# Kernel optimization log

Hardware: AMD Instinct MI355X
Metric: run time of the kernel (lower is better)

## Reference

```python
import jax, jax.numpy as jnp
import numpy as np

N_NODES = 200000
N_EDGES = 800000
N_GRAPHS = 2048
N_SUB = 32768
E_SUB = 131072
F_IN = 38
H0, H1, H2 = 256, 128, 64
BN_EPS = 1e-5


def _l2norm(x):
    n = jnp.sqrt(jnp.sum(x * x, axis=1, keepdims=True))
    return x / jnp.maximum(n, 1e-12)


def _bn(x):
    # fresh nn.BatchNorm1d in training mode: gamma=1, beta=0, biased var
    m = x.mean(0, keepdims=True)
    v = x.var(0, keepdims=True)
    return (x - m) * jax.lax.rsqrt(v + BN_EPS)


def _seg_bn(x, seg, num_seg):
    # per-subgraph BatchNorm (source loops over subgraphs, BN stats per subgraph)
    ones = jnp.ones((x.shape[0],), x.dtype)
    cnt = jnp.maximum(jax.ops.segment_sum(ones, seg, num_seg), 1.0)[:, None]
    m = jax.ops.segment_sum(x, seg, num_seg) / cnt
    v = jax.ops.segment_sum(x * x, seg, num_seg) / cnt - m * m
    return (x - m[seg]) * jax.lax.rsqrt(jnp.maximum(v[seg], 0.0) + BN_EPS)


def _seg_mean(x, seg, num_seg):
    ones = jnp.ones((x.shape[0],), x.dtype)
    cnt = jnp.maximum(jax.ops.segment_sum(ones, seg, num_seg), 1.0)[:, None]
    return jax.ops.segment_sum(x, seg, num_seg) / cnt


def _gcn(x, W, b, src, dst):
    N = x.shape[0]
    h = x @ W
    deg = jnp.ones((N,), x.dtype).at[dst].add(1.0)  # in-degree + self loop
    dinv = jax.lax.rsqrt(deg)
    coef = (dinv[src] * dinv[dst])[:, None]
    agg = jnp.zeros_like(h).at[dst].add(coef * h[src]) + (dinv * dinv)[:, None] * h
    return agg + b


def setup_inputs() -> dict:
    key = jax.random.key(0)
    ks = jax.random.split(key, 40)

    def lin(k, fi, fo):
        return jax.random.normal(k, (fi, fo), jnp.float32) / np.float32(np.sqrt(fi))

    inp = {}
    inp['x'] = jax.random.normal(ks[0], (N_NODES, F_IN), jnp.float32)
    inp['edge_index'] = jax.random.randint(ks[1], (2, N_EDGES), 0, N_NODES)
    inp['batch'] = jnp.sort(jax.random.randint(ks[2], (N_NODES,), 0, N_GRAPHS))
    inp['target_x'] = jax.random.normal(ks[3], (N_GRAPHS, F_IN), jnp.float32)
    inp['pos_x'] = jax.random.normal(ks[4], (N_SUB, F_IN), jnp.float32)
    inp['pos_edge_index'] = jax.random.randint(ks[5], (2, E_SUB), 0, N_SUB)
    inp['pos_batch'] = jnp.sort(jax.random.randint(ks[6], (N_SUB,), 0, N_GRAPHS))
    inp['neg_x'] = jax.random.normal(ks[7], (N_SUB, F_IN), jnp.float32)
    inp['neg_edge_index'] = jax.random.randint(ks[8], (2, E_SUB), 0, N_SUB)
    inp['neg_batch'] = jnp.sort(jax.random.randint(ks[9], (N_SUB,), 0, N_GRAPHS))

    # main GCN encoder
    inp['enc_W0'] = lin(ks[10], F_IN, H0); inp['enc_b0'] = jnp.zeros((H0,), jnp.float32)
    inp['enc_W1'] = lin(ks[11], H0, H1);  inp['enc_b1'] = jnp.zeros((H1,), jnp.float32)
    inp['enc_W2'] = lin(ks[12], H1, H2);  inp['enc_b2'] = jnp.zeros((H2,), jnp.float32)
    # decoder (bias=False)
    inp['dec_W0'] = lin(ks[13], H2, H1)
    inp['dec_W1'] = lin(ks[14], H1, H0)
    inp['dec_W2'] = lin(ks[15], H0, F_IN)
    # node MLP encoder
    inp['node_W0'] = lin(ks[16], F_IN, H0); inp['node_b0'] = jnp.zeros((H0,), jnp.float32)
    inp['node_W1'] = lin(ks[17], H0, H1);  inp['node_b1'] = jnp.zeros((H1,), jnp.float32)
    inp['node_W2'] = lin(ks[18], H1, H2);  inp['node_b2'] = jnp.zeros((H2,), jnp.float32)
    # subgraph GCN encoder (last layer of encode_subgraph reuses self.encoders[-1])
    inp['sub_W0'] = lin(ks[19], F_IN, H0); inp['sub_b0'] = jnp.zeros((H0,), jnp.float32)
    inp['sub_W1'] = lin(ks[20], H0, H1);  inp['sub_b1'] = jnp.zeros((H1,), jnp.float32)
    # classifier
    inp['cls_W0'] = lin(ks[21], H2, H1);  inp['cls_b0'] = jnp.zeros((H1,), jnp.float32)
    inp['cls_W1'] = lin(ks[22], H1, 16);  inp['cls_b1'] = jnp.zeros((16,), jnp.float32)
    inp['cls_W2'] = lin(ks[23], 16, 1);   inp['cls_b2'] = jnp.zeros((1,), jnp.float32)
    return inp


def reference(x, edge_index, batch, target_x, pos_x, pos_edge_index, pos_batch,
              neg_x, neg_edge_index, neg_batch,
              enc_W0, enc_b0, enc_W1, enc_b1, enc_W2, enc_b2,
              dec_W0, dec_W1, dec_W2,
              node_W0, node_b0, node_W1, node_b1, node_W2, node_b2,
              sub_W0, sub_b0, sub_W1, sub_b1,
              cls_W0, cls_b0, cls_W1, cls_b1, cls_W2, cls_b2):
    relu = jax.nn.relu
    src, dst = edge_index[0], edge_index[1]

    # encode: GCN -> ReLU -> BN (x2), GCN, L2 normalize
    h = _bn(relu(_gcn(x, enc_W0, enc_b0, src, dst)))
    h = _bn(relu(_gcn(h, enc_W1, enc_b1, src, dst)))
    z = _l2norm(_gcn(h, enc_W2, enc_b2, src, dst))

    # decode: Linear(no bias) ReLU stack, sigmoid output
    r = relu(z @ dec_W0)
    r = relu(r @ dec_W1)
    x_recon = jax.nn.sigmoid(r @ dec_W2)

    z_pool = _seg_mean(z, batch, N_GRAPHS)

    # encode_node on target node features
    t = _bn(relu(target_x @ node_W0 + node_b0))
    t = _bn(relu(t @ node_W1 + node_b1))
    target_z = _l2norm(t @ node_W2 + node_b2)

    # batched subgraph encoding: GCN stack with per-subgraph BatchNorm;
    # last layer reuses main encoders[-1] weights (as in source encode_subgraph)
    def encode_sub(sx, sei, seg):
        s, d = sei[0], sei[1]
        sh = _seg_bn(relu(_gcn(sx, sub_W0, sub_b0, s, d)), seg, N_GRAPHS)
        sh = _seg_bn(relu(_gcn(sh, sub_W1, sub_b1, s, d)), seg, N_GRAPHS)
        return _l2norm(_gcn(sh, enc_W2, enc_b2, s, d))

    pos_z = encode_sub(pos_x, pos_edge_index, pos_batch)
    pos_pool = _seg_mean(pos_z, pos_batch, N_GRAPHS)
    neg_z = encode_sub(neg_x, neg_edge_index, neg_batch)
    neg_pool = _seg_mean(neg_z, neg_batch, N_GRAPHS)

    # classify negative subgraph pools
    p = relu(neg_pool @ cls_W0 + cls_b0)
    p = relu(p @ cls_W1 + cls_b1)
    neg_pred = jax.nn.sigmoid(p @ cls_W2 + cls_b2)

    return (x_recon, z_pool, target_z, pos_pool, neg_pool, neg_pred)
```

## Files before the change

### kernel.cpp

```cpp
#include <hip/hip_runtime.h>
#include <hip/hip_bf16.h>
#include <math.h>

#define N_NODES  200000
#define N_EDGES  800000
#define N_GRAPHS 2048
#define N_SUB    32768
#define E_SUB    131072
#define F_IN     38
#define H0       256
#define H1       128
#define H2       64
#define BN_EPS   1e-5f

typedef __hip_bfloat16 bf16;
typedef __attribute__((ext_vector_type(8))) short short8;
typedef __attribute__((ext_vector_type(4))) short short4v;
typedef __attribute__((ext_vector_type(4))) float float4v;

static __host__ __device__ inline int cdiv(int a, int b) { return (a + b - 1) / b; }

__device__ inline float ldf(const float* p, size_t i) { return p[i]; }
__device__ inline float ldf(const bf16* p, size_t i)  { return __bfloat162float(p[i]); }
__device__ inline void  stf(float* p, size_t i, float v) { p[i] = v; }
// ... 248 lines not shown
__global__ __launch_bounds__(256) void k_gather6(
    const bf16* __restrict__ h, const float* __restrict__ dinv,
    const int* __restrict__ rowptr, const int* __restrict__ col,
    TO* __restrict__ o, int n, const float* __restrict__ bias, int relu)
{
    const int W = LPR * 8;
    const int NG = 64 / LPR;
    const int g = threadIdx.x / LPR;
    const int c0 = (threadIdx.x % LPR) * 8;
    const int nA = (blockIdx.x * 4 + threadIdx.y) * (2 * NG) + g * 2;
    const int nB = nA + 1;
    if (nA >= n) return;
    const bool okB = nB < n;

    int2 rp = *(const int2*)(rowptr + nA);
    int peB = okB ? rowptr[nB + 1] : rp.y;
    float diA = dinv[nA];
    float diB = okB ? dinv[nB] : 0.f;
    short8 zed = {0, 0, 0, 0, 0, 0, 0, 0};
    short8 slA = *(const short8*)(h + (size_t)nA * W + c0);
    short8 slB = okB ? *(const short8*)(h + (size_t)nB * W + c0) : zed;

    int pA = rp.x, peA = rp.y;
    int pB = rp.y;

    float accA[8], accB[8];
    float qA = diA * diA, qB = diB * diB;
#pragma unroll
    for (int j = 0; j < 8; ++j) {
        accA[j] = qA * bits2f(slA[j]);
        accB[j] = qB * bits2f(slB[j]);
    }

    int sA1 = 0, sB1 = 0;
    float dA0 = 0.f, dB0 = 0.f;
    short8 vA0 = zed, vB0 = zed;
    if (pA < peA) {
        int s0 = col[pA];
        sA1 = (pA + 1 < peA) ? col[pA + 1] : 0;
        dA0 = dinv[s0];
        vA0 = *(const short8*)(h + (size_t)s0 * W + c0);
    }
    if (pB < peB) {
        int s0 = col[pB];
        sB1 = (pB + 1 < peB) ? col[pB + 1] : 0;
        dB0 = dinv[s0];
        vB0 = *(const short8*)(h + (size_t)s0 * W + c0);
    }

    while (__any(pA < peA || pB < peB)) {
        if (pA < peA) {
            int sA2 = (pA + 2 < peA) ? col[pA + 2] : 0;
            short8 vA1 = zed;
            float dA1 = 0.f;
            if (pA + 1 < peA) {
                vA1 = *(const short8*)(h + (size_t)sA1 * W + c0);
                dA1 = dinv[sA1];
            }
            float cf = dA0 * diA;
#pragma unroll
            for (int j = 0; j < 8; ++j) accA[j] += cf * bits2f(vA0[j]);
            vA0 = vA1; dA0 = dA1; sA1 = sA2; ++pA;
        }
        if (pB < peB) {
            int sB2 = (pB + 2 < peB) ? col[pB + 2] : 0;
            short8 vB1 = zed;
            float dB1 = 0.f;
            if (pB + 1 < peB) {
                vB1 = *(const short8*)(h + (size_t)sB1 * W + c0);
                dB1 = dinv[sB1];
            }
            float cf = dB0 * diB;
#pragma unroll
            for (int j = 0; j < 8; ++j) accB[j] += cf * bits2f(vB0[j]);
            vB0 = vB1; dB0 = dB1; sB1 = sB2; ++pB;
        }
    }

    float bv[8];
#pragma unroll
    for (int j = 0; j < 8; ++j) bv[j] = 0.f;
    if (bias) {
        float4 b0 = *(const float4*)(bias + c0);
        float4 b1 = *(const float4*)(bias + c0 + 4);
        bv[0] = b0.x; bv[1] = b0.y; bv[2] = b0.z; bv[3] = b0.w;
        bv[4] = b1.x; bv[5] = b1.y; bv[6] = b1.z; bv[7] = b1.w;
    }

    auto store_row = [&](int node, float* acc) {
        float r[8];
#pragma unroll
        for (int j = 0; j < 8; ++j) {
            r[j] = acc[j] + bv[j];
            if (relu) r[j] = fmaxf(r[j], 0.f);
        }
        size_t off = (size_t)node * W + c0;
        if constexpr (sizeof(TO) == 2) {
            short8 pk;
#pragma unroll
            for (int j = 0; j < 8; ++j) pk[j] = bf16bits(r[j]);
            *(short8*)((bf16*)o + off) = pk;
        } else {
            float4 f0 = {r[0], r[1], r[2], r[3]};
            float4 f1 = {r[4], r[5], r[6], r[7]};
            *(float4*)((float*)o + off) = f0;
            *(float4*)((float*)o + off + 4) = f1;
        }
    };
    store_row(nA, accA);
    if (okB) store_row(nB, accB);
}

template <typename TO>
static void launch_gather6(const bf16* h, const float* dinv, const int* rowptr,
                           const int* col, TO* o, int n, int W,
                           const float* bias, int relu, hipStream_t stream) {
    dim3 b(64, 4);
    if (W == 128)
        k_gather6<TO, 16><<<cdiv(n, 32), b, 0, stream>>>(h, dinv, rowptr, col, o, n,
                                                         bias, relu);
    else
        k_gather6<TO, 8><<<cdiv(n, 64), b, 0, stream>>>(h, dinv, rowptr, col, o, n,
                                                        bias, relu);
}

template <int K, int M, int Mp>
__device__ inline void wpack1(const float* __restrict__ W, bf16* __restrict__ o, int j) {
    int kk = j & 31;
    int rem = j >> 5;
    int ncol = rem % Mp;
    int s = rem / Mp;
    int k = s * 32 + kk;
    float v = (k < K && ncol < M) ? W[(size_t)k * M + ncol] : 0.f;
    o[j] = __float2bfloat16(v);
}

__global__ void k_wpack_all(const float* __restrict__ eW0, const float* __restrict__ eW1,
                            const float* __restrict__ eW2, const float* __restrict__ dW0,
                            const float* __restrict__ dW1, const float* __restrict__ dW2,
                            const float* __restrict__ sW0, const float* __restrict__ sW1,
                            bf16* __restrict__ arena) {
    for (int i = blockIdx.x * 256 + threadIdx.x; i < 159744; i += gridDim.x * 256) {
        if (i < 16384)       wpack1<38, 256, 256>(eW0, arena, i);
        else if (i < 49152)  wpack1<256, 128, 128>(eW1, arena + 16384, i - 16384);
        else if (i < 57344)  wpack1<128, 64, 64>(eW2, arena + 49152, i - 49152);
        else if (i < 65536)  wpack1<64, 128, 128>(dW0, arena + 57344, i - 57344);
        else if (i < 98304)  wpack1<128, 256, 256>(dW1, arena + 65536, i - 65536);
        else if (i < 110592) wpack1<256, 38, 48>(dW2, arena + 98304, i - 98304);
        else if (i < 126976) wpack1<38, 256, 256>(sW0, arena + 110592, i - 110592);
        else                 wpack1<256, 128, 128>(sW1, arena + 126976, i - 126976);
    }
}

template <typename TC, int NT, int BNM>
__global__ __launch_bounds__(256) void k_mfma_gemm(
    const bf16* __restrict__ A, const bf16* __restrict__ Wb,
    TC* __restrict__ C, int n, int SA, int Mp, int M, int MC,
    const float* __restrict__ bias, int act,
    const float* __restrict__ mu, const float* __restrict__ sc,
    const int* __restrict__ seg)
{
    const int lane = threadIdx.x;
    const int wave = threadIdx.y;
    const int row0 = blockIdx.x * 64 + wave * 16;
    const int qr = lane >> 4;
    const int lc = lane & 15;

    float4v acc[NT];
#pragma unroll
    for (int t = 0; t < NT; ++t) acc[t] = (float4v){0.f, 0.f, 0.f, 0.f};

    size_t bnbase = 0;
    if (BNM == 2) bnbase = (size_t)seg[row0 + lc] * SA;

    const int S = SA >> 5;
    const bf16* arow = A + (size_t)(row0 + lc) * SA + qr * 8;
    const bf16* wrow = Wb + (size_t)lc * 32 + qr * 8;

    for (int s = 0; s < S; ++s) {
        short8 af = *(const short8*)(arow + s * 32);
        if (BNM != 0) {
            int kb = s * 32 + qr * 8;
            const float* mp = mu + bnbase + kb;
            const float* sp = sc + bnbase + kb;
            float4 m0 = *(const float4*)mp, m1 = *(const float4*)(mp + 4);
            float4 s0 = *(const float4*)sp, s1 = *(const float4*)(sp + 4);
            float av[8];
#pragma unroll
            for (int j = 0; j < 8; ++j) av[j] = bits2f(af[j]);
            av[0] = (av[0] - m0.x) * s0.x; av[1] = (av[1] - m0.y) * s0.y;
            av[2] = (av[2] - m0.z) * s0.z; av[3] = (av[3] - m0.w) * s0.w;
            av[4] = (av[4] - m1.x) * s1.x; av[5] = (av[5] - m1.y) * s1.y;
            av[6] = (av[6] - m1.z) * s1.z; av[7] = (av[7] - m1.w) * s1.w;
#pragma unroll
            for (int j = 0; j < 8; ++j) af[j] = bf16bits(av[j]);
        }
#pragma unroll
        for (int t = 0; t < NT; ++t) {
            short8 bfr = *(const short8*)(wrow + ((size_t)s * Mp + t * 16) * 32);
            acc[t] = __builtin_amdgcn_mfma_f32_16x16x32_bf16(bfr, af, acc[t], 0, 0, 0);
        }
    }

    const int row = row0 + lc;
#pragma unroll
    for (int t = 0; t < NT; ++t) {
        int c0 = t * 16 + qr * 4;
        if (c0 >= M) continue;
        float v[4];
#pragma unroll
        for (int r = 0; r < 4; ++r) v[r] = acc[t][r];
        if (bias) {
            if (c0 + 3 < M) {
                float4 bv = *(const float4*)(bias + c0);
                v[0] += bv.x; v[1] += bv.y; v[2] += bv.z; v[3] += bv.w;
            } else {
#pragma unroll
                for (int r = 0; r < 4; ++r) if (c0 + r < M) v[r] += bias[c0 + r];
            }
        }
#pragma unroll
        for (int r = 0; r < 4; ++r) {
            if (act == 1) v[r] = fmaxf(v[r], 0.f);
            else if (act == 2) v[r] = 1.f / (1.f + expf(-v[r]));
        }
        if (c0 + 3 < M) {
            if constexpr (sizeof(TC) == 2) {
                short4v pk = {bf16bits(v[0]), bf16bits(v[1]), bf16bits(v[2]), bf16bits(v[3])};
                *(short4v*)((bf16*)C + (size_t)row * MC + c0) = pk;
            } else {
                stf2((float*)C, ((size_t)row * MC + c0) >> 1, make_float2(v[0], v[1]));
                stf2((float*)C, ((size_t)row * MC + c0 + 2) >> 1, make_float2(v[2], v[3]));
            }
        } else {
#pragma unroll
            for (int r = 0; r < 4; ++r)
                if (c0 + r < M) stf(C, (size_t)row * MC + c0 + r, v[r]);
        }
    }
}

template <typename TC, int BNM>
static void launch_mfma(const bf16* A, const bf16* Wb, TC* C, int n, int SA,
                        int Mp, int M, int MC, const float* bias, int act,
                        const float* mu, const float* sc, const int* seg,
                        hipStream_t stream) {
    dim3 b(64, 4);
    int g = n / 64;
    if (Mp == 256)      k_mfma_gemm<TC, 16, BNM><<<g, b, 0, stream>>>(A, Wb, C, n, SA, Mp, M, MC, bias, act, mu, sc, seg);
    else if (Mp == 128) k_mfma_gemm<TC, 8, BNM><<<g, b, 0, stream>>>(A, Wb, C, n, SA, Mp, M, MC, bias, act, mu, sc, seg);
    else if (Mp == 64)  k_mfma_gemm<TC, 4, BNM><<<g, b, 0, stream>>>(A, Wb, C, n, SA, Mp, M, MC, bias, act, mu, sc, seg);
    else                k_mfma_gemm<TC, 3, BNM><<<g, b, 0, stream>>>(A, Wb, C, n, SA, Mp, M, MC, bias, act, mu, sc, seg);
}

__global__ __launch_bounds__(256) void k_decoder(
    const bf16* __restrict__ zb, const bf16* __restrict__ dW0b,
    const bf16* __restrict__ dW1b, const bf16* __restrict__ dW2b,
    float* __restrict__ xrec, int n)
{
    __shared__ __attribute__((aligned(16))) char lds[4][12288];
    const int lane = threadIdx.x;
    const int wave = threadIdx.y;
    const int lc = lane & 15, qr = lane >> 4;
    const int row0 = blockIdx.x * 64 + wave * 16;
    char* r1 = lds[wave];
    char* r2 = lds[wave] + 4096;
    const int swz = (lc & 7) << 4;

    float4v a1[8];
#pragma unroll
    for (int t = 0; t < 8; ++t) a1[t] = (float4v){0.f, 0.f, 0.f, 0.f};
    const bf16* arow = zb + (size_t)(row0 + lc) * 64 + qr * 8;
#pragma unroll
    for (int s = 0; s < 2; ++s) {
        short8 af = *(const short8*)(arow + s * 32);
#pragma unroll
        for (int t = 0; t < 8; ++t) {
            short8 wf = *(const short8*)(dW0b + ((size_t)(s * 128 + t * 16 + lc)) * 32 + qr * 8);
            a1[t] = __builtin_amdgcn_mfma_f32_16x16x32_bf16(wf, af, a1[t], 0, 0, 0);
        }
    }
#pragma unroll
    for (int t = 0; t < 8; ++t) {
        short4v pk = {bf16bits(fmaxf(a1[t][0], 0.f)), bf16bits(fmaxf(a1[t][1], 0.f)),
                      bf16bits(fmaxf(a1[t][2], 0.f)), bf16bits(fmaxf(a1[t][3], 0.f))};
        int off = lc * 256 + t * 32 + qr * 8;
        *(short4v*)(r1 + (off ^ swz)) = pk;
    }

    float4v a2[16];
#pragma unroll
    for (int t = 0; t < 16; ++t) a2[t] = (float4v){0.f, 0.f, 0.f, 0.f};
#pragma unroll
    for (int s = 0; s < 4; ++s) {
        int off = lc * 256 + s * 64 + qr * 16;
        short8 af = *(const short8*)(r1 + (off ^ swz));
#pragma unroll
        for (int t = 0; t < 16; ++t) {
            short8 wf = *(const short8*)(dW1b + ((size_t)(s * 256 + t * 16 + lc)) * 32 + qr * 8);
            a2[t] = __builtin_amdgcn_mfma_f32_16x16x32_bf16(wf, af, a2[t], 0, 0, 0);
        }
    }
#pragma unroll
    for (int t = 0; t < 16; ++t) {
        short4v pk = {bf16bits(fmaxf(a2[t][0], 0.f)), bf16bits(fmaxf(a2[t][1], 0.f)),
                      bf16bits(fmaxf(a2[t][2], 0.f)), bf16bits(fmaxf(a2[t][3], 0.f))};
        int off = lc * 512 + t * 32 + qr * 8;
        *(short4v*)(r2 + (off ^ swz)) = pk;
    }

    float4v a3[3];
#pragma unroll
    for (int t = 0; t < 3; ++t) a3[t] = (float4v){0.f, 0.f, 0.f, 0.f};
#pragma unroll
    for (int s = 0; s < 8; ++s) {
        int off = lc * 512 + s * 64 + qr * 16;
        short8 af = *(const short8*)(r2 + (off ^ swz));
#pragma unroll
        for (int t = 0; t < 3; ++t) {
            short8 wf = *(const short8*)(dW2b + ((size_t)(s * 48 + t * 16 + lc)) * 32 + qr * 8);
            a3[t] = __builtin_amdgcn_mfma_f32_16x16x32_bf16(wf, af, a3[t], 0, 0, 0);
        }
    }
    float* orow = xrec + (size_t)(row0 + lc) * 38;
#pragma unroll
    for (int t = 0; t < 3; ++t) {
        int c0 = t * 16 + qr * 4;
        float v0 = 1.f / (1.f + expf(-a3[t][0]));
        float v1 = 1.f / (1.f + expf(-a3[t][1]));
        float v2 = 1.f / (1.f + expf(-a3[t][2]));
        float v3 = 1.f / (1.f + expf(-a3[t][3]));
        if (c0 + 1 < 38) *(float2*)(orow + c0) = make_float2(v0, v1);
        if (c0 + 3 < 38) *(float2*)(orow + c0 + 2) = make_float2(v2, v3);
    }
}

template <typename TA, typename TC, int NJ>
__global__ __launch_bounds__(256) void k_gemm(
    const TA* __restrict__ A, const float* __restrict__ W,
    TC* __restrict__ C, int n, int K, int M,
    const float* __restrict__ bias, int act,
    const float* __restrict__ mu, const float* __restrict__ sc)
{
    __shared__ float alds[64 * 32];
    __shared__ float wlds[32 * 256];
    const int l = threadIdx.x;
    const int wy = threadIdx.y;
    const int tid = wy * 64 + l;
    const int row0 = blockIdx.x * 64;

    float acc[16][NJ];
#pragma unroll
    for (int r = 0; r < 16; ++r)
#pragma unroll
        for (int j = 0; j < NJ; ++j) acc[r][j] = 0.f;

    int cidx[NJ]; bool jval[NJ];
#pragma unroll
    for (int j = 0; j < NJ; ++j) {
        cidx[j] = l + 64 * j;
        jval[j] = cidx[j] < M;
    }

    for (int k0 = 0; k0 < K; k0 += 32) {
        int kt = min(32, K - k0);
        __syncthreads();
        for (int i = tid; i < 64 * 32; i += 256) {
            int r = i >> 5, kk = i & 31;
            int row = row0 + r, k = k0 + kk;
            float v = (row < n && k < K) ? ldf(A, (size_t)row * K + k) : 0.f;
            if (mu && k < K) v = (v - mu[k]) * sc[k];
            alds[i] = v;
        }
        for (int i = tid; i < kt * M; i += 256)
            wlds[i] = W[(size_t)k0 * M + i];
        if (kt < 32)
            for (int i = kt * M + tid; i < 32 * M; i += 256) wlds[i] = 0.f;
        __syncthreads();

#pragma unroll 2
        for (int kkg = 0; kkg < 8; ++kkg) {
            float wv[4][NJ];
#pragma unroll
            for (int q = 0; q < 4; ++q)
#pragma unroll
                for (int j = 0; j < NJ; ++j)
                    wv[q][j] = jval[j] ? wlds[(kkg * 4 + q) * M + cidx[j]] : 0.f;
#pragma unroll
            for (int rr = 0; rr < 16; ++rr) {
                const float4* arow = (const float4*)&alds[(wy * 16 + rr) * 32];
                float4 av = arow[kkg];
#pragma unroll
                for (int j = 0; j < NJ; ++j) {
                    acc[rr][j] += av.x * wv[0][j];
                    acc[rr][j] += av.y * wv[1][j];
                    acc[rr][j] += av.z * wv[2][j];
                    acc[rr][j] += av.w * wv[3][j];
                }
            }
        }
    }

#pragma unroll
    for (int rr = 0; rr < 16; ++rr) {
        int row = row0 + wy * 16 + rr;
// ... 61 lines not shown
    if (c < M) {
        float m = sum[c] / (float)n;
        float v = fmaxf(sumsq[c] / (float)n - m * m, 0.f);
        sum[c] = m;
        sumsq[c] = rsqrtf(v + BN_EPS);
    }
}

template <int CPL>
__global__ __launch_bounds__(256) void k_segbn(
    const bf16* __restrict__ x, const int* __restrict__ gstart, int nseg,
    float* __restrict__ mu, float* __restrict__ sc)
{
    const int M = 64 * CPL;
    int s = blockIdx.x * 4 + threadIdx.y;
    if (s >= nseg) return;
    int l = threadIdx.x;
    int gs = gstart[s], ge = gstart[s + 1];
    float sum[CPL], sq[CPL];
#pragma unroll
    for (int j = 0; j < CPL; ++j) { sum[j] = 0.f; sq[j] = 0.f; }
    for (int r = gs; r < ge; ++r) {
        const bf16* px = x + (size_t)r * M + l * CPL;
        if constexpr (CPL == 4) {
            short4v v4 = *(const short4v*)px;
#pragma unroll
            for (int j = 0; j < 4; ++j) {
                float v = bits2f(v4[j]);
                sum[j] += v; sq[j] += v * v;
            }
        } else {
            __hip_bfloat162 v2 = *(const __hip_bfloat162*)px;
            float v0 = __bfloat162float(v2.x), v1 = __bfloat162float(v2.y);
            sum[0] += v0; sq[0] += v0 * v0;
            sum[1] += v1; sq[1] += v1 * v1;
        }
    }
    float c = fmaxf((float)(ge - gs), 1.f);
#pragma unroll
    for (int j = 0; j < CPL; ++j) {
        float m = sum[j] / c;
        float v = fmaxf(sq[j] / c - m * m, 0.f);
        mu[(size_t)s * M + l * CPL + j] = m;
        sc[(size_t)s * M + l * CPL + j] = rsqrtf(v + BN_EPS);
    }
}

__global__ __launch_bounds__(256) void k_pool(
    const float* __restrict__ z, const int* __restrict__ gstart, int nseg,
    float* __restrict__ o)
{
    int s = blockIdx.x * 4 + threadIdx.y;
    if (s >= nseg) return;
    int l = threadIdx.x;
    int gs = gstart[s], ge = gstart[s + 1];
    float acc = 0.f;
    for (int r = gs; r < ge; ++r) acc += z[(size_t)r * 64 + l];
    o[(size_t)s * 64 + l] = acc / fmaxf((float)(ge - gs), 1.f);
}

__global__ __launch_bounds__(256) void k_l2pool(
    const float* __restrict__ zs, const int* __restrict__ gstart, int nseg,
    float* __restrict__ o)
{
    int s = blockIdx.x * 4 + threadIdx.y;
    if (s >= nseg) return;
    int l = threadIdx.x;
    int gs = gstart[s], ge = gstart[s + 1];
    float acc = 0.f;
    for (int r = gs; r < ge; ++r) {
        float v = zs[(size_t)r * 64 + l];
        float ss = v * v;
        for (int off = 32; off > 0; off >>= 1) ss += __shfl_xor(ss, off, 64);
        acc += v / fmaxf(sqrtf(ss), 1e-12f);
    }
    o[(size_t)s * 64 + l] = acc / fmaxf((float)(ge - gs), 1.f);
}

__global__ void k_l2norm2(float* __restrict__ x, bf16* __restrict__ xb, int n) {
    int row = blockIdx.x * 4 + threadIdx.y;
    if (row >= n) return;
    int l = threadIdx.x;
    float v = x[(size_t)row * 64 + l];
    float ss = v * v;
    for (int o = 32; o > 0; o >>= 1) ss += __shfl_xor(ss, o, 64);
    float r = v / fmaxf(sqrtf(ss), 1e-12f);
    x[(size_t)row * 64 + l] = r;
    if (xb) xb[(size_t)row * 64 + l] = __float2bfloat16(r);
}

template <typename TA, typename TC>
static void launch_gemm(const TA* A, const float* W, TC* C, int n, int K, int M,
                        const float* bias, int act, const float* mu, const float* sc,
                        hipStream_t stream) {
    dim3 b(64, 4);
    int g = cdiv(n, 64);
    int nj = (M + 63) >> 6;
    if (nj >= 4)      k_gemm<TA, TC, 4><<<g, b, 0, stream>>>(A, W, C, n, K, M, bias, act, mu, sc);
    else if (nj == 2) k_gemm<TA, TC, 2><<<g, b, 0, stream>>>(A, W, C, n, K, M, bias, act, mu, sc);
    else              k_gemm<TA, TC, 1><<<g, b, 0, stream>>>(A, W, C, n, K, M, bias, act, mu, sc);
}

extern "C" void kernel_launch(void* const* d_in, const int* in_sizes, int n_in,
                              void* d_out, int out_size, void* d_ws, size_t ws_size,
                              hipStream_t stream) {
    const float* x        = (const float*)d_in[0];
    const int*   ei       = (const int*)  d_in[1];
    const int*   batch    = (const int*)  d_in[2];
    const float* target_x = (const float*)d_in[3];
    const float* pos_x    = (const float*)d_in[4];
    const int*   pos_ei   = (const int*)  d_in[5];
    const int*   pos_b    = (const int*)  d_in[6];
    const float* neg_x    = (const float*)d_in[7];
    const int*   neg_ei   = (const int*)  d_in[8];
    const int*   neg_b    = (const int*)  d_in[9];
    const float* enc_W0 = (const float*)d_in[10]; const float* enc_b0 = (const float*)d_in[11];
    const float* enc_W1 = (const float*)d_in[12]; const float* enc_b1 = (const float*)d_in[13];
    const float* enc_W2 = (const float*)d_in[14]; const float* enc_b2 = (const float*)d_in[15];
    const float* dec_W0 = (const float*)d_in[16];
    const float* dec_W1 = (const float*)d_in[17];
    const float* dec_W2 = (const float*)d_in[18];
    const float* node_W0 = (const float*)d_in[19]; const float* node_b0 = (const float*)d_in[20];
    const float* node_W1 = (const float*)d_in[21]; const float* node_b1 = (const float*)d_in[22];
    const float* node_W2 = (const float*)d_in[23]; const float* node_b2 = (const float*)d_in[24];
    const float* sub_W0 = (const float*)d_in[25]; const float* sub_b0 = (const float*)d_in[26];
    const float* sub_W1 = (const float*)d_in[27]; const float* sub_b1 = (const float*)d_in[28];
    const float* cls_W0 = (const float*)d_in[29]; const float* cls_b0 = (const float*)d_in[30];
    const float* cls_W1 = (const float*)d_in[31]; const float* cls_b1 = (const float*)d_in[32];
    const float* cls_W2 = (const float*)d_in[33]; const float* cls_b2 = (const float*)d_in[34];

    float* out = (float*)d_out;
    const size_t OFF_XREC  = 0;
    const size_t OFF_ZPOOL = (size_t)N_NODES * F_IN;
    const size_t OFF_TZ    = OFF_ZPOOL + (size_t)N_GRAPHS * H2;
    const size_t OFF_PPOOL = OFF_TZ    + (size_t)N_GRAPHS * H2;
    const size_t OFF_NPOOL = OFF_PPOOL + (size_t)N_GRAPHS * H2;
    const size_t OFF_PRED  = OFF_NPOOL + (size_t)N_GRAPHS * H2;

    char* wsp = (char*)d_ws;
    auto alloc = [&](size_t nfloats) -> float* {
        float* p = (float*)wsp;
        wsp += ((nfloats + 63) / 64) * 64 * sizeof(float);
        return p;
    };
    float* R1     = alloc((size_t)N_NODES * 128);
    float* R2     = alloc((size_t)N_NODES * 128);
    float* dinv   = alloc(N_NODES);
    int*   cnt    = (int*)alloc(N_NODES);
    int*   rowptr = (int*)alloc(N_NODES + 1);
    int*   bsum   = (int*)alloc(1024);
    int*   ccol   = (int*)alloc(N_EDGES);
    float* ssum   = alloc(256);
    float* ssumsq = alloc(256);
    bf16*  wpk    = (bf16*)alloc(80 * 1024);
    (void)ws_size; (void)in_sizes; (void)n_in; (void)out_size;

    bf16* eW0b = wpk;
    bf16* eW1b = eW0b + 16384;
    bf16* eW2b = eW1b + 32768;
    bf16* dW0b = eW2b + 8192;
    bf16* dW1b = dW0b + 8192;
    bf16* dW2b = dW1b + 32768;
    bf16* sW0b = dW2b + 12288;
    bf16* sW1b = sW0b + 16384;

    float* tailf    = R2 + (size_t)16 * 1024 * 1024;
    float* segsumM  = tailf;
    float* segsumqM = tailf + (size_t)1048576;
    float* mx       = tailf + (size_t)2097152;
    int*   msrc     = (int*)(mx + (size_t)2 * N_SUB * F_IN);
    int*   mdst     = msrc + 2 * E_SUB;
    int*   mb       = mdst + 2 * E_SUB;
    int*   gstartM  = mb + 2 * N_SUB;
    int*   gstart2k = gstartM + 4112;

    dim3 b64x4(64, 4);
    auto zero = [&](void* p, size_t nfloats) {
        k_zero<<<cdiv((int)nfloats, 256), 256, 0, stream>>>((float*)p, (int)nfloats);
    };

    k_wpack_all<<<624, 256, 0, stream>>>(enc_W0, enc_W1, enc_W2, dec_W0, dec_W1,
                                         dec_W2, sub_W0, sub_W1, wpk);

    auto build_graph = [&](const int* srcp, const int* dstp, int n, int e) {
        zero(cnt, n);
        k_count<<<cdiv(e, 256), 256, 0, stream>>>(dstp, cnt, e);
        k_dinv<<<cdiv(n, 256), 256, 0, stream>>>(cnt, dinv, n);
        int nb = cdiv(n, 256);
        k_scan_sum<<<nb, 256, 0, stream>>>(cnt, bsum, n);
        k_scan_top<<<1, 1024, 0, stream>>>(bsum, nb);
        k_scan_apply<<<nb, 256, 0, stream>>>(cnt, bsum, rowptr, n);
        zero(cnt, n);
        k_fill<<<cdiv(e, 256), 256, 0, stream>>>(srcp, dstp, rowptr, cnt, ccol, e);
    };

    auto bn_stats = [&](auto* xx, int n, int M) {
        zero(ssum, 512);
        int rpb = 256 / (M >> 3);
        int g = min(320, cdiv(n, rpb));
        k_bn_stats8<<<g, 256, 0, stream>>>(xx, n, M, ssum, ssumsq);
        k_bn_fin<<<1, 256, 0, stream>>>(ssum, ssumsq, n, M);
    };

    build_graph(ei, ei + N_EDGES, N_NODES, N_EDGES);

    bf16* Y0 = (bf16*)R2;
    launch_gather<float, bf16>(x, dinv, rowptr, ccol, Y0, N_NODES, F_IN, 64,
                               nullptr, 0, stream);
    bf16* a0 = (bf16*)R1;
    launch_mfma<bf16, 0>(Y0, eW0b, a0, N_NODES, 64, 256, H0, H0, enc_b0, 1,
                         nullptr, nullptr, nullptr, stream);
    bn_stats(a0, N_NODES, H0);

    bf16* G1 = (bf16*)R2;
    launch_mfma<bf16, 1>(a0, eW1b, G1, N_NODES, 256, 128, H1, H1, nullptr, 0,
                         ssum, ssumsq, nullptr, stream);
    bf16* a1 = (bf16*)R1;
    launch_gather6<bf16>(G1, dinv, rowptr, ccol, a1, N_NODES, 128, enc_b1, 1, stream);
    bn_stats(a1, N_NODES, H1);

    bf16* G2 = (bf16*)R2;
    launch_mfma<bf16, 1>(a1, eW2b, G2, N_NODES, 128, 64, H2, H2, nullptr, 0,
                         ssum, ssumsq, nullptr, stream);
    float* z  = R1;
    bf16*  zb = (bf16*)(R1 + (size_t)N_NODES * 64);
    launch_gather6<float>(G2, dinv, rowptr, ccol, z, N_NODES, 64, enc_b2, 0, stream);
    k_l2norm2<<<cdiv(N_NODES, 4), b64x4, 0, stream>>>(z, zb, N_NODES);

    k_gbound<<<cdiv(N_NODES, 256), 256, 0, stream>>>(batch, N_NODES, N_GRAPHS, gstart2k);
    k_pool<<<cdiv(N_GRAPHS, 4), b64x4, 0, stream>>>(z, gstart2k, N_GRAPHS,
                                                    out + OFF_ZPOOL);

    k_decoder<<<N_NODES / 64, b64x4, 0, stream>>>(zb, dW0b, dW1b, dW2b,
                                                  out + OFF_XREC, N_NODES);

    float* t0 = R2;
    launch_gemm<float, float>(target_x, node_W0, t0, N_GRAPHS, F_IN, H0, node_b0, 1,
                              nullptr, nullptr, stream);
    bn_stats(t0, N_GRAPHS, H0);
    float* t1 = R1;
    launch_gemm<float, float>(t0, node_W1, t1, N_GRAPHS, H0, H1, node_b1, 1,
                              ssum, ssumsq, stream);
    bn_stats(t1, N_GRAPHS, H1);
    launch_gemm<float, float>(t1, node_W2, out + OFF_TZ, N_GRAPHS, H1, H2, node_b2, 0,
                              ssum, ssumsq, stream);
    k_l2norm2<<<cdiv(N_GRAPHS, 4), b64x4, 0, stream>>>(out + OFF_TZ, nullptr, N_GRAPHS);

    k_merge<<<2048, 256, 0, stream>>>(pos_x, neg_x, pos_ei, neg_ei, pos_b, neg_b,
                                      mx, msrc, mdst, mb);
    const int NS2 = 2 * N_SUB, ES2 = 2 * E_SUB, NG2 = 2 * N_GRAPHS;
    build_graph(msrc, mdst, NS2, ES2);
    k_gbound<<<cdiv(NS2, 256), 256, 0, stream>>>(mb, NS2, NG2, gstartM);

    bf16* Ys = (bf16*)R2;
    launch_gather<float, bf16>(mx, dinv, rowptr, ccol, Ys, NS2, F_IN, 64,
                               nullptr, 0, stream);
    bf16* as0 = (bf16*)R1;
    launch_mfma<bf16, 0>(Ys, sW0b, as0, NS2, 64, 256, H0, H0, sub_b0, 1,
                         nullptr, nullptr, nullptr, stream);
    k_segbn<4><<<cdiv(NG2, 4), b64x4, 0, stream>>>(as0, gstartM, NG2,
                                                   segsumM, segsumqM);

    bf16* Gs1 = (bf16*)R2;
    launch_mfma<bf16, 2>(as0, sW1b, Gs1, NS2, 256, 128, H1, H1, nullptr, 0,
                         segsumM, segsumqM, mb, stream);
    bf16* as1 = (bf16*)R1;
    launch_gather6<bf16>(Gs1, dinv, rowptr, ccol, as1, NS2, 128, sub_b1, 1, stream);
    k_segbn<2><<<cdiv(NG2, 4), b64x4, 0, stream>>>(as1, gstartM, NG2,
                                                   segsumM, segsumqM);

    bf16* Gs2 = (bf16*)R2;
    launch_mfma<bf16, 2>(as1, eW2b, Gs2, NS2, 128, 64, H2, H2, nullptr, 0,
                         segsumM, segsumqM, mb, stream);
    float* zs = R1;
    launch_gather6<float>(Gs2, dinv, rowptr, ccol, zs, NS2, 64, enc_b2, 0, stream);
    k_l2pool<<<cdiv(NG2, 4), b64x4, 0, stream>>>(zs, gstartM, NG2, out + OFF_PPOOL);

    float* c1 = R2;
    launch_gemm<float, float>(out + OFF_NPOOL, cls_W0, c1, N_GRAPHS, H2, H1, cls_b0, 1,
                              nullptr, nullptr, stream);
    float* c2 = R1;
    launch_gemm<float, float>(c1, cls_W1, c2, N_GRAPHS, H1, 16, cls_b1, 1,
                              nullptr, nullptr, stream);
    launch_gemm<float, float>(c2, cls_W2, out + OFF_PRED, N_GRAPHS, 16, 1, cls_b2, 2,
                              nullptr, nullptr, stream);
}
```

Baseline: 1.271 ms.

## Fold BatchNorm into GEMM weights and pipeline multi-tile MFMA GEMM

Result: slower. 1.334 ms (+5.0%).

```diff
diff --git a/kernel.cpp b/kernel.cpp
--- a/kernel.cpp
+++ b/kernel.cpp
@@ -424,79 +424,110 @@
     }
 }
 
-template <typename TC, int NT, int BNM>
+template <int K, int M, int Mp>
+__global__ void k_wfold(const float* __restrict__ W, const float* __restrict__ mu,
+                        const float* __restrict__ sc, bf16* __restrict__ Wb,
+                        float* __restrict__ bout) {
+    const int tot = (K / 32) * Mp * 32;
+    for (int i = blockIdx.x * 256 + threadIdx.x; i < tot; i += gridDim.x * 256) {
+        int kk = i & 31;
+        int rem = i >> 5;
+        int ncol = rem % Mp;
+        int s = rem / Mp;
+        int k = s * 32 + kk;
+        float v = (k < K && ncol < M) ? sc[k] * W[(size_t)k * M + ncol] : 0.f;
+        Wb[i] = __float2bfloat16(v);
+    }
+    if (blockIdx.x == 0 && threadIdx.x < M) {
+        int j = threadIdx.x;
+        float s = 0.f;
+        for (int k = 0; k < K; ++k) s -= mu[k] * sc[k] * W[(size_t)k * M + j];
+        bout[j] = s;
+    }
+}
+
+template <typename TC, int NT, int S, int BNM, int TPB>
 __global__ __launch_bounds__(256) void k_mfma_gemm(
     const bf16* __restrict__ A, const bf16* __restrict__ Wb,
-    TC* __restrict__ C, int n, int SA, int Mp, int M, int MC,
+    TC* __restrict__ C, int ntiles, int M, int MC,
     const float* __restrict__ bias, int act,
     const float* __restrict__ mu, const float* __restrict__ sc,
     const int* __restrict__ seg)
 {
+    const int SA = S * 32;
+    const int Mp = NT * 16;
     const int lane = threadIdx.x;
     const int wave = threadIdx.y;
-    const int row0 = blockIdx.x * 64 + wave * 16;
     const int qr = lane >> 4;
     const int lc = lane & 15;
-
-    float4v acc[NT];
-#pragma unroll
-    for (int t = 0; t < NT; ++t) acc[t] = (float4v){0.f, 0.f, 0.f, 0.f};
-
-    size_t bnbase = 0;
-    if (BNM == 2) bnbase = (size_t)seg[row0 + lc] * SA;
-
-    const int S = SA >> 5;
-    const bf16* arow = A + (size_t)(row0 + lc) * SA + qr * 8;
-    const bf16* wrow = Wb + (size_t)lc * 32 + qr * 8;
-
-    for (int s = 0; s < S; ++s) {
-        short8 af = *(const short8*)(arow + s * 32);
-        if (BNM != 0) {
-            int kb = s * 32 + qr * 8;
-            const float* mp = mu + bnbase + kb;
-            const float* sp = sc + bnbase + kb;
-            float4 m0 = *(const float4*)mp, m1 = *(const float4*)(mp + 4);
-            float4 s0 = *(const float4*)sp, s1 = *(const float4*)(sp + 4);
-            float av[8];
-#pragma unroll
-            for (int j = 0; j < 8; ++j) av[j] = bits2f(af[j]);
-            av[0] = (av[0] - m0.x) * s0.x; av[1] = (av[1] - m0.y) * s0.y;
-            av[2] = (av[2] - m0.z) * s0.z; av[3] = (av[3] - m0.w) * s0.w;
-            av[4] = (av[4] - m1.x) * s1.x; av[5] = (av[5] - m1.y) * s1.y;
-            av[6] = (av[6] - m1.z) * s1.z; av[7] = (av[7] - m1.w) * s1.w;
-#pragma unroll
-            for (int j = 0; j < 8; ++j) af[j] = bf16bits(av[j]);
-        }
+    const int tile0 = blockIdx.x * TPB;
+    const int ntl = min(TPB, ntiles - tile0);
+    const bf16* wbase = Wb + (size_t)lc * 32 + qr * 8;
+
+    short8 cur[S], nxt[S];
+    {
+        const bf16* ar = A + (size_t)(tile0 * 64 + wave * 16 + lc) * SA + qr * 8;
+#pragma unroll
+        for (int s = 0; s < S; ++s) cur[s] = *(const short8*)(ar + s * 32);
+    }
+
+    for (int it = 0; it < ntl; ++it) {
+        const int row0 = (tile0 + it) * 64 + wave * 16;
+        if (it + 1 < ntl) {
+            const bf16* ar = A + (size_t)(row0 + 64 + lc) * SA + qr * 8;
+#pragma unroll
+            for (int s = 0; s < S; ++s) nxt[s] = *(const short8*)(ar + s * 32);
+        }
+        if (BNM == 2) {
+            size_t bnbase = (size_t)seg[row0 + lc] * SA;
+#pragma unroll
+            for (int s = 0; s < S; ++s) {
+                int kb = s * 32 + qr * 8;
+                const float* mp = mu + bnbase + kb;
+                const float* sp = sc + bnbase + kb;
+                float4 m0 = *(const float4*)mp, m1 = *(const float4*)(mp + 4);
+                float4 s0 = *(const float4*)sp, s1 = *(const float4*)(sp + 4);
+                float av[8];
+#pragma unroll
+                for (int j = 0; j < 8; ++j) av[j] = bits2f(cur[s][j]);
+                av[0] = (av[0] - m0.x) * s0.x; av[1] = (av[1] - m0.y) * s0.y;
+                av[2] = (av[2] - m0.z) * s0.z; av[3] = (av[3] - m0.w) * s0.w;
+                av[4] = (av[4] - m1.x) * s1.x; av[5] = (av[5] - m1.y) * s1.y;
+                av[6] = (av[6] - m1.z) * s1.z; av[7] = (av[7] - m1.w) * s1.w;
+#pragma unroll
+                for (int j = 0; j < 8; ++j) cur[s][j] = bf16bits(av[j]);
+            }
+        }
+
+        float4v acc[NT];
+#pragma unroll
+        for (int t = 0; t < NT; ++t) acc[t] = (float4v){0.f, 0.f, 0.f, 0.f};
+#pragma unroll
+        for (int s = 0; s < S; ++s) {
+#pragma unroll
+            for (int t = 0; t < NT; ++t) {
+                short8 wf = *(const short8*)(wbase + ((size_t)s * Mp + t * 16) * 32);
+                acc[t] = __builtin_amdgcn_mfma_f32_16x16x32_bf16(wf, cur[s], acc[t], 0, 0, 0);
+            }
+        }
+
+        const int row = row0 + lc;
 #pragma unroll
         for (int t = 0; t < NT; ++t) {
-            short8 bfr = *(const short8*)(wrow + ((size_t)s * Mp + t * 16) * 32);
-            acc[t] = __builtin_amdgcn_mfma_f32_16x16x32_bf16(bfr, af, acc[t], 0, 0, 0);
-        }
-    }
-
-    const int row = row0 + lc;
-#pragma unroll
-    for (int t = 0; t < NT; ++t) {
-        int c0 = t * 16 + qr * 4;
-        if (c0 >= M) continue;
-        float v[4];
-#pragma unroll
-        for (int r = 0; r < 4; ++r) v[r] = acc[t][r];
-        if (bias) {
-            if (c0 + 3 < M) {
+            int c0 = t * 16 + qr * 4;
+            if (c0 >= M) continue;
+            float v[4];
+#pragma unroll
+            for (int r = 0; r < 4; ++r) v[r] = acc[t][r];
+            if (bias) {
                 float4 bv = *(const float4*)(bias + c0);
                 v[0] += bv.x; v[1] += bv.y; v[2] += bv.z; v[3] += bv.w;
-            } else {
-#pragma unroll
-                for (int r = 0; r < 4; ++r) if (c0 + r < M) v[r] += bias[c0 + r];
             }
-        }
-#pragma unroll
-        for (int r = 0; r < 4; ++r) {
-            if (act == 1) v[r] = fmaxf(v[r], 0.f);
-            else if (act == 2) v[r] = 1.f / (1.f + expf(-v[r]));
-        }
-        if (c0 + 3 < M) {
+#pragma unroll
+            for (int r = 0; r < 4; ++r) {
+                if (act == 1) v[r] = fmaxf(v[r], 0.f);
+                else if (act == 2) v[r] = 1.f / (1.f + expf(-v[r]));
+            }
             if constexpr (sizeof(TC) == 2) {
                 short4v pk = {bf16bits(v[0]), bf16bits(v[1]), bf16bits(v[2]), bf16bits(v[3])};
                 *(short4v*)((bf16*)C + (size_t)row * MC + c0) = pk;
@@ -504,11 +535,9 @@
                 stf2((float*)C, ((size_t)row * MC + c0) >> 1, make_float2(v[0], v[1]));
                 stf2((float*)C, ((size_t)row * MC + c0 + 2) >> 1, make_float2(v[2], v[3]));
             }
-        } else {
-#pragma unroll
-            for (int r = 0; r < 4; ++r)
-                if (c0 + r < M) stf(C, (size_t)row * MC + c0 + r, v[r]);
-        }
+        }
+#pragma unroll
+        for (int s = 0; s < S; ++s) cur[s] = nxt[s];
     }
 }
 
@@ -518,11 +547,24 @@
                         const float* mu, const float* sc, const int* seg,
                         hipStream_t stream) {
     dim3 b(64, 4);
-    int g = n / 64;
-    if (Mp == 256)      k_mfma_gemm<TC, 16, BNM><<<g, b, 0, stream>>>(A, Wb, C, n, SA, Mp, M, MC, bias, act, mu, sc, seg);
-    else if (Mp == 128) k_mfma_gemm<TC, 8, BNM><<<g, b, 0, stream>>>(A, Wb, C, n, SA, Mp, M, MC, bias, act, mu, sc, seg);
-    else if (Mp == 64)  k_mfma_gemm<TC, 4, BNM><<<g, b, 0, stream>>>(A, Wb, C, n, SA, Mp, M, MC, bias, act, mu, sc, seg);
-    else                k_mfma_gemm<TC, 3, BNM><<<g, b, 0, stream>>>(A, Wb, C, n, SA, Mp, M, MC, bias, act, mu, sc, seg);
+    int ntiles = n / 64;
+    if (ntiles >= 2000) {
+        int g = cdiv(ntiles, 4);
+        if (SA == 64 && Mp == 256)
+            k_mfma_gemm<TC, 16, 2, BNM, 4><<<g, b, 0, stream>>>(A, Wb, C, ntiles, M, MC, bias, act, mu, sc, seg);
+        else if (SA == 256 && Mp == 128)
+            k_mfma_gemm<TC, 8, 8, BNM, 4><<<g, b, 0, stream>>>(A, Wb, C, ntiles, M, MC, bias, act, mu, sc, seg);
+        else if (SA == 128 && Mp == 64)
+            k_mfma_gemm<TC, 4, 4, BNM, 4><<<g, b, 0, stream>>>(A, Wb, C, ntiles, M, MC, bias, act, mu, sc, seg);
+    } else {
+        int g = cdiv(ntiles, 2);
+        if (SA == 64 && Mp == 256)
+            k_mfma_gemm<TC, 16, 2, BNM, 2><<<g, b, 0, stream>>>(A, Wb, C, ntiles, M, MC, bias, act, mu, sc, seg);
+        else if (SA == 256 && Mp == 128)
+            k_mfma_gemm<TC, 8, 8, BNM, 2><<<g, b, 0, stream>>>(A, Wb, C, ntiles, M, MC, bias, act, mu, sc, seg);
+        else if (SA == 128 && Mp == 64)
+            k_mfma_gemm<TC, 4, 4, BNM, 2><<<g, b, 0, stream>>>(A, Wb, C, ntiles, M, MC, bias, act, mu, sc, seg);
+    }
 }
 
 __global__ __launch_bounds__(256) void k_decoder(
@@ -890,7 +932,8 @@
     int*   ccol   = (int*)alloc(N_EDGES);
     float* ssum   = alloc(256);
     float* ssumsq = alloc(256);
-    bf16*  wpk    = (bf16*)alloc(80 * 1024);
+    bf16*  wpk    = (bf16*)alloc(101 * 1024);
+    float* bfold  = alloc(256);
     (void)ws_size; (void)in_sizes; (void)n_in; (void)out_size;
 
     bf16* eW0b = wpk;
@@ -901,6 +944,8 @@
     bf16* dW2b = dW1b + 32768;
     bf16* sW0b = dW2b + 12288;
     bf16* sW1b = sW0b + 16384;
+    bf16* fW1b = sW1b + 32768;
+    bf16* fW2b = fW1b + 32768;
 
     float* tailf    = R2 + (size_t)16 * 1024 * 1024;
     float* segsumM  = tailf;
@@ -935,7 +980,7 @@
     auto bn_stats = [&](auto* xx, int n, int M) {
         zero(ssum, 512);
         int rpb = 256 / (M >> 3);
-        int g = min(320, cdiv(n, rpb));
+        int g = min(512, cdiv(n, rpb));
         k_bn_stats8<<<g, 256, 0, stream>>>(xx, n, M, ssum, ssumsq);
         k_bn_fin<<<1, 256, 0, stream>>>(ssum, ssumsq, n, M);
     };
@@ -949,17 +994,19 @@
     launch_mfma<bf16, 0>(Y0, eW0b, a0, N_NODES, 64, 256, H0, H0, enc_b0, 1,
                          nullptr, nullptr, nullptr, stream);
     bn_stats(a0, N_NODES, H0);
+    k_wfold<256, 128, 128><<<128, 256, 0, stream>>>(enc_W1, ssum, ssumsq, fW1b, bfold);
 
     bf16* G1 = (bf16*)R2;
-    launch_mfma<bf16, 1>(a0, eW1b, G1, N_NODES, 256, 128, H1, H1, nullptr, 0,
-                         ssum, ssumsq, nullptr, stream);
+    launch_mfma<bf16, 0>(a0, fW1b, G1, N_NODES, 256, 128, H1, H1, bfold, 0,
+                         nullptr, nullptr, nullptr, stream);
     bf16* a1 = (bf16*)R1;
     launch_gather6<bf16>(G1, dinv, rowptr, ccol, a1, N_NODES, 128, enc_b1, 1, stream);
     bn_stats(a1, N_NODES, H1);
+    k_wfold<128, 64, 64><<<32, 256, 0, stream>>>(enc_W2, ssum, ssumsq, fW2b, bfold + 128);
 
     bf16* G2 = (bf16*)R2;
-    launch_mfma<bf16, 1>(a1, eW2b, G2, N_NODES, 128, 64, H2, H2, nullptr, 0,
-                         ssum, ssumsq, nullptr, stream);
+    launch_mfma<bf16, 0>(a1, fW2b, G2, N_NODES, 128, 64, H2, H2, bfold + 128, 0,
+                         nullptr, nullptr, nullptr, stream);
     float* z  = R1;
     bf16*  zb = (bf16*)(R1 + (size_t)N_NODES * 64);
     launch_gather6<float>(G2, dinv, rowptr, ccol, z, N_NODES, 64, enc_b2, 0, stream);
```

## Fold BatchNorm into next-layer weights and fuse layer-0/1 GEMMs via recompute

Applied to the files above, without the earlier changes.

New measurement: 1.207 ms. -5.0%, faster.

```diff
diff --git a/kernel.cpp b/kernel.cpp
--- a/kernel.cpp
+++ b/kernel.cpp
@@ -424,6 +424,28 @@
     }
 }
 
+template <int K, int M, int Mp>
+__global__ void k_wfold(const float* __restrict__ W, const float* __restrict__ mu,
+                        const float* __restrict__ sc, bf16* __restrict__ Wb,
+                        float* __restrict__ bout) {
+    const int tot = (K / 32) * Mp * 32;
+    for (int i = blockIdx.x * 256 + threadIdx.x; i < tot; i += gridDim.x * 256) {
+        int kk = i & 31;
+        int rem = i >> 5;
+        int ncol = rem % Mp;
+        int s = rem / Mp;
+        int k = s * 32 + kk;
+        float v = (k < K && ncol < M) ? sc[k] * W[(size_t)k * M + ncol] : 0.f;
+        Wb[i] = __float2bfloat16(v);
+    }
+    if (blockIdx.x == 0 && threadIdx.x < M) {
+        int j = threadIdx.x;
+        float s = 0.f;
+        for (int k = 0; k < K; ++k) s -= mu[k] * sc[k] * W[(size_t)k * M + j];
+        bout[j] = s;
+    }
+}
+
 template <typename TC, int NT, int BNM>
 __global__ __launch_bounds__(256) void k_mfma_gemm(
     const bf16* __restrict__ A, const bf16* __restrict__ Wb,
@@ -523,6 +545,135 @@
     else if (Mp == 128) k_mfma_gemm<TC, 8, BNM><<<g, b, 0, stream>>>(A, Wb, C, n, SA, Mp, M, MC, bias, act, mu, sc, seg);
     else if (Mp == 64)  k_mfma_gemm<TC, 4, BNM><<<g, b, 0, stream>>>(A, Wb, C, n, SA, Mp, M, MC, bias, act, mu, sc, seg);
     else                k_mfma_gemm<TC, 3, BNM><<<g, b, 0, stream>>>(A, Wb, C, n, SA, Mp, M, MC, bias, act, mu, sc, seg);
+}
+
+__global__ __launch_bounds__(256) void k_l0stats(
+    const bf16* __restrict__ Y0, const bf16* __restrict__ W0b,
+    const float* __restrict__ b0, float* __restrict__ sum,
+    float* __restrict__ sumsq, int ntiles)
+{
+    __shared__ float ls[4][512];
+    const int lane = threadIdx.x;
+    const int wave = threadIdx.y;
+    const int lc = lane & 15, qr = lane >> 4;
+
+    float bv[16];
+#pragma unroll
+    for (int t = 0; t < 16; ++t) bv[t] = b0[t * 16 + lc];
+
+    float sReg[16], qReg[16];
+#pragma unroll
+    for (int t = 0; t < 16; ++t) { sReg[t] = 0.f; qReg[t] = 0.f; }
+
+    for (int tile = blockIdx.x; tile < ntiles; tile += gridDim.x) {
+        const int row0 = tile * 64 + wave * 16;
+        const bf16* arow = Y0 + (size_t)(row0 + lc) * 64 + qr * 8;
+        float4v acc[16];
+#pragma unroll
+        for (int t = 0; t < 16; ++t) acc[t] = (float4v){0.f, 0.f, 0.f, 0.f};
+#pragma unroll
+        for (int s = 0; s < 2; ++s) {
+            short8 af = *(const short8*)(arow + s * 32);
+#pragma unroll
+            for (int t = 0; t < 16; ++t) {
+                short8 wf = *(const short8*)(W0b + ((size_t)(s * 256 + t * 16 + lc)) * 32 + qr * 8);
+                acc[t] = __builtin_amdgcn_mfma_f32_16x16x32_bf16(af, wf, acc[t], 0, 0, 0);
+            }
+        }
+#pragma unroll
+        for (int t = 0; t < 16; ++t) {
+            float s4 = 0.f, q4 = 0.f;
+#pragma unroll
+            for (int r = 0; r < 4; ++r) {
+                float v = fmaxf(acc[t][r] + bv[t], 0.f);
+                v = bits2f(bf16bits(v));
+                s4 += v;
+                q4 += v * v;
+            }
+            s4 += __shfl_xor(s4, 16, 64); s4 += __shfl_xor(s4, 32, 64);
+            q4 += __shfl_xor(q4, 16, 64); q4 += __shfl_xor(q4, 32, 64);
+            sReg[t] += s4;
+            qReg[t] += q4;
+        }
+    }
+    if (lane < 16) {
+#pragma unroll
+        for (int t = 0; t < 16; ++t) {
+            ls[wave][t * 16 + lc] = sReg[t];
+            ls[wave][256 + t * 16 + lc] = qReg[t];
+        }
+    }
+    __syncthreads();
+    int tid = wave * 64 + lane;
+    if (tid < 256) {
+        atomicAdd(&sum[tid], ls[0][tid] + ls[1][tid] + ls[2][tid] + ls[3][tid]);
+        atomicAdd(&sumsq[tid],
+                  ls[0][256 + tid] + ls[1][256 + tid] + ls[2][256 + tid] + ls[3][256 + tid]);
+    }
+}
+
+__global__ __launch_bounds__(256) void k_fused01(
+    const bf16* __restrict__ Y0, const bf16* __restrict__ W0b,
+    const float* __restrict__ b0, const bf16* __restrict__ W1b,
+    const float* __restrict__ b1f, bf16* __restrict__ G1, int n)
+{
+    __shared__ __attribute__((aligned(16))) char lds[4][8192];
+    const int lane = threadIdx.x;
+    const int wave = threadIdx.y;
+    const int lc = lane & 15, qr = lane >> 4;
+    const int row0 = blockIdx.x * 64 + wave * 16;
+    char* r2 = lds[wave];
+    const int swz = (lc & 7) << 4;
+
+    {
+        float4v acc[16];
+#pragma unroll
+        for (int t = 0; t < 16; ++t) acc[t] = (float4v){0.f, 0.f, 0.f, 0.f};
+        const bf16* arow = Y0 + (size_t)(row0 + lc) * 64 + qr * 8;
+#pragma unroll
+        for (int s = 0; s < 2; ++s) {
+            short8 af = *(const short8*)(arow + s * 32);
+#pragma unroll
+            for (int t = 0; t < 16; ++t) {
+                short8 wf = *(const short8*)(W0b + ((size_t)(s * 256 + t * 16 + lc)) * 32 + qr * 8);
+                acc[t] = __builtin_amdgcn_mfma_f32_16x16x32_bf16(wf, af, acc[t], 0, 0, 0);
+            }
+        }
+#pragma unroll
+        for (int t = 0; t < 16; ++t) {
+            int c0 = t * 16 + qr * 4;
+            float4 bv = *(const float4*)(b0 + c0);
+            short4v pk = {bf16bits(fmaxf(acc[t][0] + bv.x, 0.f)),
+                          bf16bits(fmaxf(acc[t][1] + bv.y, 0.f)),
+                          bf16bits(fmaxf(acc[t][2] + bv.z, 0.f)),
+                          bf16bits(fmaxf(acc[t][3] + bv.w, 0.f))};
+            int off = lc * 512 + t * 32 + qr * 8;
+            *(short4v*)(r2 + (off ^ swz)) = pk;
+        }
+    }
+
+    float4v a2[8];
+#pragma unroll
+    for (int t = 0; t < 8; ++t) a2[t] = (float4v){0.f, 0.f, 0.f, 0.f};
+#pragma unroll
+    for (int s = 0; s < 8; ++s) {
+        int off = lc * 512 + s * 64 + qr * 16;
+        short8 af = *(const short8*)(r2 + (off ^ swz));
+#pragma unroll
+        for (int t = 0; t < 8; ++t) {
+            short8 wf = *(const short8*)(W1b + ((size_t)(s * 128 + t * 16 + lc)) * 32 + qr * 8);
+            a2[t] = __builtin_amdgcn_mfma_f32_16x16x32_bf16(wf, af, a2[t], 0, 0, 0);
+        }
+    }
+    const int row = row0 + lc;
+#pragma unroll
+    for (int t = 0; t < 8; ++t) {
+        int c0 = t * 16 + qr * 4;
+        float4 bv = *(const float4*)(b1f + c0);
+        short4v pk = {bf16bits(a2[t][0] + bv.x), bf16bits(a2[t][1] + bv.y),
+                      bf16bits(a2[t][2] + bv.z), bf16bits(a2[t][3] + bv.w)};
+        *(short4v*)(G1 + (size_t)row * 128 + c0) = pk;
+    }
 }
 
 __global__ __launch_bounds__(256) void k_decoder(
@@ -890,7 +1041,8 @@
     int*   ccol   = (int*)alloc(N_EDGES);
     float* ssum   = alloc(256);
     float* ssumsq = alloc(256);
-    bf16*  wpk    = (bf16*)alloc(80 * 1024);
+    bf16*  wpk    = (bf16*)alloc(101 * 1024);
+    float* bfold  = alloc(256);
     (void)ws_size; (void)in_sizes; (void)n_in; (void)out_size;
 
     bf16* eW0b = wpk;
@@ -901,6 +1053,8 @@
     bf16* dW2b = dW1b + 32768;
     bf16* sW0b = dW2b + 12288;
     bf16* sW1b = sW0b + 16384;
+    bf16* fW1b = sW1b + 32768;
+    bf16* fW2b = fW1b + 32768;
 
     float* tailf    = R2 + (size_t)16 * 1024 * 1024;
     float* segsumM  = tailf;
@@ -935,31 +1089,35 @@
     auto bn_stats = [&](auto* xx, int n, int M) {
         zero(ssum, 512);
         int rpb = 256 / (M >> 3);
-        int g = min(320, cdiv(n, rpb));
+        int g = min(512, cdiv(n, rpb));
         k_bn_stats8<<<g, 256, 0, stream>>>(xx, n, M, ssum, ssumsq);
         k_bn_fin<<<1, 256, 0, stream>>>(ssum, ssumsq, n, M);
     };
 
     build_graph(ei, ei + N_EDGES, N_NODES, N_EDGES);
 
-    bf16* Y0 = (bf16*)R2;
+    bf16* Y0 = (bf16*)R1;
     launch_gather<float, bf16>(x, dinv, rowptr, ccol, Y0, N_NODES, F_IN, 64,
                                nullptr, 0, stream);
-    bf16* a0 = (bf16*)R1;
-    launch_mfma<bf16, 0>(Y0, eW0b, a0, N_NODES, 64, 256, H0, H0, enc_b0, 1,
-                         nullptr, nullptr, nullptr, stream);
-    bn_stats(a0, N_NODES, H0);
+
+    zero(ssum, 512);
+    k_l0stats<<<512, b64x4, 0, stream>>>(Y0, eW0b, enc_b0, ssum, ssumsq,
+                                         N_NODES / 64);
+    k_bn_fin<<<1, 256, 0, stream>>>(ssum, ssumsq, N_NODES, H0);
+    k_wfold<256, 128, 128><<<128, 256, 0, stream>>>(enc_W1, ssum, ssumsq, fW1b, bfold);
 
     bf16* G1 = (bf16*)R2;
-    launch_mfma<bf16, 1>(a0, eW1b, G1, N_NODES, 256, 128, H1, H1, nullptr, 0,
-                         ssum, ssumsq, nullptr, stream);
+    k_fused01<<<N_NODES / 64, b64x4, 0, stream>>>(Y0, eW0b, enc_b0, fW1b, bfold,
+                                                  G1, N_NODES);
+
     bf16* a1 = (bf16*)R1;
     launch_gather6<bf16>(G1, dinv, rowptr, ccol, a1, N_NODES, 128, enc_b1, 1, stream);
     bn_stats(a1, N_NODES, H1);
+    k_wfold<128, 64, 64><<<32, 256, 0, stream>>>(enc_W2, ssum, ssumsq, fW2b, bfold + 128);
 
     bf16* G2 = (bf16*)R2;
-    launch_mfma<bf16, 1>(a1, eW2b, G2, N_NODES, 128, 64, H2, H2, nullptr, 0,
-                         ssum, ssumsq, nullptr, stream);
+    launch_mfma<bf16, 0>(a1, fW2b, G2, N_NODES, 128, 64, H2, H2, bfold + 128, 0,
+                         nullptr, nullptr, nullptr, stream);
     float* z  = R1;
     bf16*  zb = (bf16*)(R1 + (size_t)N_NODES * 64);
     launch_gather6<float>(G2, dinv, rowptr, ccol, z, N_NODES, 64, enc_b2, 0, stream);
```
